# Kernel optimization log

Measured on AMD Instinct MI355X. Metric: run time of the kernel, lower is better.

Reference implementation:

```python
import jax, jax.numpy as jnp
import numpy as np

LMAX = 2
C = 128            # uniform multiplicity per degree
H = 128            # hidden channels
M = (LMAX + 1) ** 2  # 9 spherical coefficients
EPS = 1e-6


def _pack_indices():
    # flat layout per degree block: [mul, 2l+1] channel-major; packed layout: [coeff, channel]
    pack = np.zeros(M * C, dtype=np.int64)
    offset = 0
    for l in range(LMAX + 1):
        dim = 2 * l + 1
        for m in range(dim):
            coeff = l * l + m
            for c in range(C):
                pack[coeff * C + c] = offset + c * dim + m
        offset += C * dim
    unpack = np.argsort(pack)
    return jnp.asarray(pack), jnp.asarray(unpack)

PACK_IDX, UNPACK_IDX = _pack_indices()
# expand_index: degree index for each of the M coefficients
EXPAND_IDX = jnp.asarray(np.repeat(np.arange(LMAX + 1), 2 * np.arange(LMAX + 1) + 1))


def setup_inputs() -> dict:
    key = jax.random.key(0)
    ks = jax.random.split(key, 6)
    N = 10000
    A = 42  # (2*(lmax+1)) * (2*(lmax+1)+1) = 6*7 flattened S2 grid points
    bound = 1.0 / np.sqrt(C)
    return {
        "x": jax.random.normal(ks[0], (N, M * C), dtype=jnp.float32),
        "norm_weight": jnp.ones((LMAX + 1, C), dtype=jnp.float32),
        "w1": jax.random.uniform(ks[1], (LMAX + 1, H, C), jnp.float32, -bound, bound),
        "b1": jnp.zeros((1, 1, H), dtype=jnp.float32),
        "grid_w": jax.random.uniform(ks[2], (2 * H, H), jnp.float32, -bound, bound),
        "grid_b": jnp.zeros((2 * H,), dtype=jnp.float32),
        "w2": jax.random.uniform(ks[3], (LMAX + 1, C, H), jnp.float32, -bound, bound),
        "b2": jnp.zeros((1, 1, C), dtype=jnp.float32),
        "to_grid_mat": jax.random.normal(ks[4], (A, M), dtype=jnp.float32) * 0.3,
        "from_grid_mat": jax.random.normal(ks[5], (M, A), dtype=jnp.float32) * 0.3,
    }


def reference(x, norm_weight, w1, b1, grid_w, grid_b, w2, b2, to_grid_mat, from_grid_mat):
    N = x.shape[0]
    # --- pack flat irreps -> [N, M, C] (pure permutation gather; no padding for uniform irreps)
    p = jnp.take(x, PACK_IDX, axis=1).reshape(N, M, C)
    # --- merged equivariant RMS norm over all (coeff, channel), per-degree-channel affine
    rms = jnp.sqrt(jnp.mean(p * p, axis=(1, 2), keepdims=True) + EPS)
    h = (p / rms) * norm_weight[EXPAND_IDX][None]  # [N, M, C]
    # --- SO3LinearFlat #1: per-degree dense C -> H, bias only on l=0 coeff
    h = jnp.einsum("nmc,mhc->nmh", h, w1[EXPAND_IDX])
    h = h.at[:, 0:1, :].add(b1)
    # --- to S2 grid: [N, M, H] -> [N, A, H]
    g = jnp.einsum("am,nmh->nah", to_grid_mat, h)
    # --- pointwise SwiGLU on grid: H -> 2H linear, silu gate
    z = jnp.einsum("nah,oh->nao", g, grid_w) + grid_b
    g = jax.nn.silu(z[..., :H]) * z[..., H:]
    # --- from S2 grid: [N, A, H] -> [N, M, H]
    h = jnp.einsum("ma,nah->nmh", from_grid_mat, g)
    # --- SO3LinearFlat #2: per-degree dense H -> C, bias only on l=0 coeff
    out = jnp.einsum("nmh,mch->nmc", h, w2[EXPAND_IDX])
    out = out.at[:, 0:1, :].add(b2)
    # --- unpack back to flat irreps layout
    return jnp.take(out.reshape(N, M * C), UNPACK_IDX, axis=1)
```

## Files before the change

### kernel.cpp

```cpp
#include <hip/hip_runtime.h>
#include <math.h>

typedef unsigned short u16;
typedef __attribute__((ext_vector_type(8))) short bf16x8;
typedef __attribute__((ext_vector_type(4))) float f32x4;
typedef __attribute__((ext_vector_type(16))) float f32x16;

constexpr int OFF_W1 = 0;
constexpr int OFF_W2 = 49152;
constexpr int OFF_GW = 98304;
constexpr int OFF_TG = 131072;
constexpr int OFF_FG = 132096;
constexpr int WS_ELEMS = 133632;

__device__ __forceinline__ u16 f2bf(float f) {
    unsigned u = __float_as_uint(f);
    u += 0x7FFFu + ((u >> 16) & 1u);
    return (u16)(u >> 16);
}

__global__ void prep_kernel(const float* __restrict__ w1, const float* __restrict__ gw,
                            const float* __restrict__ w2, const float* __restrict__ tg,
                            const float* __restrict__ fg, u16* __restrict__ wsb) {
    const int idx = blockIdx.x * blockDim.x + threadIdx.x;
    const int str = gridDim.x * blockDim.x;
    for (int i = idx; i < 49152; i += str) wsb[OFF_W1 + i] = f2bf(w1[i]);
    for (int i = idx; i < 49152; i += str) wsb[OFF_W2 + i] = f2bf(w2[i]);
    for (int i = idx; i < 32768; i += str) wsb[OFF_GW + i] = f2bf(gw[i]);
    for (int i = idx; i < 1024; i += str) {
        int a = i >> 4, k = i & 15;
        wsb[OFF_TG + i] = (a < 42 && k < 9) ? f2bf(tg[a * 9 + k]) : (u16)0;
    }
    for (int i = idx; i < 1536; i += str) {
        int m = i / 48, k = i - m * 48;
        wsb[OFF_FG + i] = (m < 9 && k < 42) ? f2bf(fg[m * 42 + k]) : (u16)0;
    }
}

__global__ __launch_bounds__(256, 2) void eqffn_mfma(
    const float* __restrict__ x, const float* __restrict__ nw,
    const float* __restrict__ b1f, const float* __restrict__ gbf,
    const float* __restrict__ b2f, const u16* __restrict__ wsb,
    float* __restrict__ out, int N)
{
    __shared__ u16 sh_a1[64 * 136];
    __shared__ u16 sh_h1T[4 * 128 * 24];
    __shared__ u16 sh_g[48 * 136];
    __shared__ u16 sh_g2T[128 * 56];
    __shared__ float sh_nw[384];
    __shared__ float sh_b1[128];
    __shared__ float sh_b2[128];
    __shared__ float sh_gb[256];

    const int tid  = threadIdx.x;
    const int w    = tid >> 6;
    const int lane = tid & 63;
    const int q    = lane >> 4;
    const int r    = lane & 15;
    const int r32  = lane & 31;
    const int half = lane >> 5;
    const int n0   = blockIdx.x * 4;

    const bf16x8 tgA0 = *(const bf16x8*)&wsb[OFF_TG + r32 * 16 + half * 8];
    const bf16x8 tgA1 = *(const bf16x8*)&wsb[OFF_TG + (32 + r32) * 16 + half * 8];
    bf16x8 fgA[3];
    #pragma unroll
    for (int k = 0; k < 3; ++k)
        fgA[k] = *(const bf16x8*)&wsb[OFF_FG + r32 * 48 + k * 16 + half * 8];
    bf16x8 gwL[2][4], gwH[2][4];
    #pragma unroll
    for (int p = 0; p < 2; ++p) {
        const int oL = (2 * w + p) * 16 + r;
        #pragma unroll
        for (int k = 0; k < 4; ++k) {
            gwL[p][k] = *(const bf16x8*)&wsb[OFF_GW + oL * 128 + k * 32 + q * 8];
            gwH[p][k] = *(const bf16x8*)&wsb[OFF_GW + (oL + 128) * 128 + k * 32 + q * 8];
        }
    }

    for (int i = tid; i < 384; i += 256) sh_nw[i] = nw[i];
    if (tid < 128) { sh_b1[tid] = b1f[tid]; sh_b2[tid] = b2f[tid]; }
    sh_gb[tid] = gbf[tid];
    {
        unsigned long long* z1 = (unsigned long long*)sh_h1T;
        for (int i = tid; i < 3072; i += 256) z1[i] = 0ull;
        unsigned long long* z2 = (unsigned long long*)sh_g2T;
        for (int i = tid; i < 1792; i += 256) z2[i] = 0ull;
    }
    __syncthreads();

    const int myn = n0 + w;
    float4 xv[5];
    float ss = 0.f;
    if (myn < N) {
        const float4* xr = (const float4*)(x + (size_t)myn * 1152);
        for (int i = lane, c2 = 0; i < 288; i += 64, ++c2) {
            float4 v = xr[i]; xv[c2] = v;
            ss += v.x * v.x + v.y * v.y + v.z * v.z + v.w * v.w;
        }
    }
    #pragma unroll
    for (int off = 32; off; off >>= 1) ss += __shfl_xor(ss, off);
    const float inv = 1.0f / sqrtf(ss * (1.0f / 1152.0f) + 1e-6f);
    if (myn < N) {
        for (int i = lane, c2 = 0; i < 288; i += 64, ++c2) {
            float4 v = xv[c2];
            #pragma unroll
            for (int e = 0; e < 4; ++e) {
                const int f = i * 4 + e;
                const float val = ((const float*)&v)[e] * inv;
                int row, c, l;
                if (f < 128)      { l = 0; c = f;            row = w; }
                else if (f < 512) { int t = f - 128; l = 1; c = t / 3; row = 16 + w * 3 + (t - c * 3); }
                else              { int t = f - 512; l = 2; c = t / 5; row = 32 + w * 5 + (t - c * 5); }
                sh_a1[row * 136 + c] = f2bf(val * sh_nw[l * 128 + c]);
            }
        }
    }
    __syncthreads();

    {
        f32x4 acc[4][2];
        #pragma unroll
        for (int a = 0; a < 4; ++a)
            #pragma unroll
            for (int b = 0; b < 2; ++b)
                #pragma unroll
                for (int e = 0; e < 4; ++e) acc[a][b][e] = 0.f;
        #pragma unroll
        for (int mt = 0; mt < 4; ++mt) {
            const int l = (mt == 0) ? 0 : ((mt == 1) ? 1 : 2);
            #pragma unroll
            for (int k = 0; k < 4; ++k) {
                bf16x8 af = *(const bf16x8*)&sh_a1[(mt * 16 + r) * 136 + k * 32 + q * 8];
                #pragma unroll
                for (int nt = 0; nt < 2; ++nt) {
                    const int h = (2 * w + nt) * 16 + r;
                    bf16x8 bf = *(const bf16x8*)&wsb[OFF_W1 + (l * 128 + h) * 128 + k * 32 + q * 8];
                    acc[mt][nt] = __builtin_amdgcn_mfma_f32_16x16x32_bf16(af, bf, acc[mt][nt], 0, 0, 0);
                }
            }
        }
        #pragma unroll
        for (int mt = 0; mt < 4; ++mt) {
            #pragma unroll
            for (int nt = 0; nt < 2; ++nt) {
                const int h = (2 * w + nt) * 16 + r;
                #pragma unroll
                for (int rg = 0; rg < 4; ++rg) {
                    const int rr = q * 4 + rg;
                    const float v = acc[mt][nt][rg];
                    if (mt == 0) {
                        if (rr < 4) sh_h1T[(rr * 128 + h) * 24 + 0] = f2bf(v + sh_b1[h]);
                    } else if (mt == 1) {
                        if (rr < 12) { int nd = rr / 3, mm = rr - nd * 3; sh_h1T[(nd * 128 + h) * 24 + 1 + mm] = f2bf(v); }
                    } else {
                        int rr2 = (mt - 2) * 16 + rr;
                        if (rr2 < 20) { int nd = rr2 / 5, mm = rr2 - nd * 5; sh_h1T[(nd * 128 + h) * 24 + 4 + mm] = f2bf(v); }
                    }
                }
            }
        }
    }
    __syncthreads();

    for (int nn = 0; nn < 4; ++nn) {
        {
            bf16x8 bfn = *(const bf16x8*)&sh_h1T[(nn * 128 + w * 32 + r32) * 24 + half * 8];
            f32x16 ac0, ac1;
            #pragma unroll
            for (int e = 0; e < 16; ++e) { ac0[e] = 0.f; ac1[e] = 0.f; }
            ac0 = __builtin_amdgcn_mfma_f32_32x32x16_bf16(tgA0, bfn, ac0, 0, 0, 0);
            ac1 = __builtin_amdgcn_mfma_f32_32x32x16_bf16(tgA1, bfn, ac1, 0, 0, 0);
            const int h = w * 32 + r32;
            #pragma unroll
            for (int rg = 0; rg < 16; ++rg) {
                const int ar = (rg & 3) + 8 * (rg >> 2) + 4 * half;
                sh_g[ar * 136 + h] = f2bf(ac0[rg]);
                const int ar1 = 32 + ar;
                if (ar1 < 48) sh_g[ar1 * 136 + h] = f2bf(ac1[rg]);
            }
        }
        __syncthreads();

        bf16x8 bfr[3][4];
        #pragma unroll
        for (int nt = 0; nt < 3; ++nt)
            #pragma unroll
            for (int k = 0; k < 4; ++k)
                bfr[nt][k] = *(const bf16x8*)&sh_g[(nt * 16 + r) * 136 + k * 32 + q * 8];
        __syncthreads();

        f32x4 aL[2][3], aH[2][3];
        #pragma unroll
        for (int p = 0; p < 2; ++p)
            #pragma unroll
            for (int nt = 0; nt < 3; ++nt)
                #pragma unroll
                for (int e = 0; e < 4; ++e) { aL[p][nt][e] = 0.f; aH[p][nt][e] = 0.f; }
        #pragma unroll
        for (int p = 0; p < 2; ++p) {
            #pragma unroll
            for (int k = 0; k < 4; ++k) {
                #pragma unroll
                for (int nt = 0; nt < 3; ++nt) {
                    aL[p][nt] = __builtin_amdgcn_mfma_f32_16x16x32_bf16(gwL[p][k], bfr[nt][k], aL[p][nt], 0, 0, 0);
                    aH[p][nt] = __builtin_amdgcn_mfma_f32_16x16x32_bf16(gwH[p][k], bfr[nt][k], aH[p][nt], 0, 0, 0);
                }
            }
        }
        #pragma unroll
        for (int p = 0; p < 2; ++p) {
            #pragma unroll
            for (int nt = 0; nt < 3; ++nt) {
                #pragma unroll
                for (int rg = 0; rg < 4; ++rg) {
                    const int o = (2 * w + p) * 16 + q * 4 + rg;
                    const int a = nt * 16 + r;
                    const float zl = aL[p][nt][rg] + sh_gb[o];
                    const float zh = aH[p][nt][rg] + sh_gb[128 + o];
                    const float gv = zl * (1.0f / (1.0f + __expf(-zl))) * zh;
                    if (a < 42) sh_g2T[o * 56 + a] = f2bf(gv);
                }
            }
        }

        {
            f32x16 ac;
            #pragma unroll
            for (int e = 0; e < 16; ++e) ac[e] = 0.f;
            const int h = w * 32 + r32;
            #pragma unroll
            for (int k = 0; k < 3; ++k) {
                bf16x8 bv = *(const bf16x8*)&sh_g2T[h * 56 + k * 16 + half * 8];
                ac = __builtin_amdgcn_mfma_f32_32x32x16_bf16(fgA[k], bv, ac, 0, 0, 0);
            }
            #pragma unroll
            for (int rg = 0; rg < 16; ++rg) {
                const int m = (rg & 3) + 8 * (rg >> 2) + 4 * half;
                if (m < 9) {
                    const int row = (m == 0) ? nn : ((m < 4) ? (16 + nn * 3 + (m - 1)) : (32 + nn * 5 + (m - 4)));
                    sh_a1[row * 136 + h] = f2bf(ac[rg]);
                }
            }
        }
    }
    __syncthreads();

    {
        f32x4 acc[4][2];
        #pragma unroll
        for (int a = 0; a < 4; ++a)
            #pragma unroll
            for (int b = 0; b < 2; ++b)
                #pragma unroll
                for (int e = 0; e < 4; ++e) acc[a][b][e] = 0.f;
        #pragma unroll
        for (int mt = 0; mt < 4; ++mt) {
            const int l = (mt == 0) ? 0 : ((mt == 1) ? 1 : 2);
            #pragma unroll
            for (int k = 0; k < 4; ++k) {
                bf16x8 af = *(const bf16x8*)&sh_a1[(mt * 16 + r) * 136 + k * 32 + q * 8];
                #pragma unroll
                for (int nt = 0; nt < 2; ++nt) {
                    const int c = (2 * w + nt) * 16 + r;
                    bf16x8 bf = *(const bf16x8*)&wsb[OFF_W2 + (l * 128 + c) * 128 + k * 32 + q * 8];
                    acc[mt][nt] = __builtin_amdgcn_mfma_f32_16x16x32_bf16(af, bf, acc[mt][nt], 0, 0, 0);
                }
            }
        }
        #pragma unroll
        for (int mt = 0; mt < 4; ++mt) {
            #pragma unroll
            for (int nt = 0; nt < 2; ++nt) {
                const int c = (2 * w + nt) * 16 + r;
                #pragma unroll
                for (int rg = 0; rg < 4; ++rg) {
                    const int rr = q * 4 + rg;
                    const float v = acc[mt][nt][rg];
                    if (mt == 0) {
                        if (rr < 4) { int gn = n0 + rr; if (gn < N) out[(size_t)gn * 1152 + c] = v + sh_b2[c]; }
                    } else if (mt == 1) {
                        if (rr < 12) { int nd = rr / 3, mm = rr - nd * 3; int gn = n0 + nd;
                                       if (gn < N) out[(size_t)gn * 1152 + 128 + c * 3 + mm] = v; }
                    } else {
                        int rr2 = (mt - 2) * 16 + rr;
                        if (rr2 < 20) { int nd = rr2 / 5, mm = rr2 - nd * 5; int gn = n0 + nd;
                                        if (gn < N) out[(size_t)gn * 1152 + 512 + c * 5 + mm] = v; }
                    }
                }
            }
        }
    }
}

extern "C" void kernel_launch(void* const* d_in, const int* in_sizes, int n_in,
                              void* d_out, int out_size, void* d_ws, size_t ws_size,
                              hipStream_t stream)
{
    const float* x  = (const float*)d_in[0];
    const float* nw = (const float*)d_in[1];
    const float* w1 = (const float*)d_in[2];
    const float* b1 = (const float*)d_in[3];
    const float* gw = (const float*)d_in[4];
    const float* gb = (const float*)d_in[5];
    const float* w2 = (const float*)d_in[6];
    const float* b2 = (const float*)d_in[7];
    const float* tg = (const float*)d_in[8];
    const float* fg = (const float*)d_in[9];
    float* out = (float*)d_out;
    u16* wsb = (u16*)d_ws;

    const int N = in_sizes[0] / 1152;
    prep_kernel<<<64, 256, 0, stream>>>(w1, gw, w2, tg, fg, wsb);
    eqffn_mfma<<<(N + 3) / 4, 256, 0, stream>>>(x, nw, b1, gb, b2, wsb, out, N);
}
```

Before: 257.1 us.

## Shrink LDS and register footprint to run three blocks per CU

Raises the launch-bounds occupancy target from 2 to 3 blocks per CU. To make that fit, the staging buffer for the first linear's output (sh_h1T) shrinks to a single node slice. The first-linear accumulators now stay in registers and one node's slice is written per loop iteration. The grid SwiGLU weights are no longer held in registers for the whole kernel; they are reloaded from global memory inside each node iteration. This trades repeated cached weight loads and a longer-lived accumulator for more concurrent waves to hide latency.

```diff
diff --git a/kernel.cpp b/kernel.cpp
--- a/kernel.cpp
+++ b/kernel.cpp
@@ -37,14 +37,14 @@
     }
 }
 
-__global__ __launch_bounds__(256, 2) void eqffn_mfma(
+__global__ __launch_bounds__(256, 3) void eqffn_mfma(
     const float* __restrict__ x, const float* __restrict__ nw,
     const float* __restrict__ b1f, const float* __restrict__ gbf,
     const float* __restrict__ b2f, const u16* __restrict__ wsb,
     float* __restrict__ out, int N)
 {
     __shared__ u16 sh_a1[64 * 136];
-    __shared__ u16 sh_h1T[4 * 128 * 24];
+    __shared__ u16 sh_h1T[128 * 20];
     __shared__ u16 sh_g[48 * 136];
     __shared__ u16 sh_g2T[128 * 56];
     __shared__ float sh_nw[384];
@@ -67,23 +67,13 @@
     #pragma unroll
     for (int k = 0; k < 3; ++k)
         fgA[k] = *(const bf16x8*)&wsb[OFF_FG + r32 * 48 + k * 16 + half * 8];
-    bf16x8 gwL[2][4], gwH[2][4];
-    #pragma unroll
-    for (int p = 0; p < 2; ++p) {
-        const int oL = (2 * w + p) * 16 + r;
-        #pragma unroll
-        for (int k = 0; k < 4; ++k) {
-            gwL[p][k] = *(const bf16x8*)&wsb[OFF_GW + oL * 128 + k * 32 + q * 8];
-            gwH[p][k] = *(const bf16x8*)&wsb[OFF_GW + (oL + 128) * 128 + k * 32 + q * 8];
-        }
-    }
 
     for (int i = tid; i < 384; i += 256) sh_nw[i] = nw[i];
     if (tid < 128) { sh_b1[tid] = b1f[tid]; sh_b2[tid] = b2f[tid]; }
     sh_gb[tid] = gbf[tid];
     {
         unsigned long long* z1 = (unsigned long long*)sh_h1T;
-        for (int i = tid; i < 3072; i += 256) z1[i] = 0ull;
+        for (int i = tid; i < 640; i += 256) z1[i] = 0ull;
         unsigned long long* z2 = (unsigned long long*)sh_g2T;
         for (int i = tid; i < 1792; i += 256) z2[i] = 0ull;
     }
@@ -119,14 +109,14 @@
     }
     __syncthreads();
 
+    f32x4 acc1[4][2];
     {
-        f32x4 acc[4][2];
         #pragma unroll
         for (int a = 0; a < 4; ++a)
             #pragma unroll
             for (int b = 0; b < 2; ++b)
                 #pragma unroll
-                for (int e = 0; e < 4; ++e) acc[a][b][e] = 0.f;
+                for (int e = 0; e < 4; ++e) acc1[a][b][e] = 0.f;
         #pragma unroll
         for (int mt = 0; mt < 4; ++mt) {
             const int l = (mt == 0) ? 0 : ((mt == 1) ? 1 : 2);
@@ -137,10 +127,13 @@
                 for (int nt = 0; nt < 2; ++nt) {
                     const int h = (2 * w + nt) * 16 + r;
                     bf16x8 bf = *(const bf16x8*)&wsb[OFF_W1 + (l * 128 + h) * 128 + k * 32 + q * 8];
-                    acc[mt][nt] = __builtin_amdgcn_mfma_f32_16x16x32_bf16(af, bf, acc[mt][nt], 0, 0, 0);
-                }
-            }
-        }
+                    acc1[mt][nt] = __builtin_amdgcn_mfma_f32_16x16x32_bf16(af, bf, acc1[mt][nt], 0, 0, 0);
+                }
+            }
+        }
+    }
+
+    for (int nn = 0; nn < 4; ++nn) {
         #pragma unroll
         for (int mt = 0; mt < 4; ++mt) {
             #pragma unroll
@@ -149,24 +142,21 @@
                 #pragma unroll
                 for (int rg = 0; rg < 4; ++rg) {
                     const int rr = q * 4 + rg;
-                    const float v = acc[mt][nt][rg];
+                    const float v = acc1[mt][nt][rg];
                     if (mt == 0) {
-                        if (rr < 4) sh_h1T[(rr * 128 + h) * 24 + 0] = f2bf(v + sh_b1[h]);
+                        if (rr == nn) sh_h1T[h * 20 + 0] = f2bf(v + sh_b1[h]);
                     } else if (mt == 1) {
-                        if (rr < 12) { int nd = rr / 3, mm = rr - nd * 3; sh_h1T[(nd * 128 + h) * 24 + 1 + mm] = f2bf(v); }
+                        if (rr >= 3 * nn && rr < 3 * nn + 3) sh_h1T[h * 20 + 1 + (rr - 3 * nn)] = f2bf(v);
                     } else {
-                        int rr2 = (mt - 2) * 16 + rr;
-                        if (rr2 < 20) { int nd = rr2 / 5, mm = rr2 - nd * 5; sh_h1T[(nd * 128 + h) * 24 + 4 + mm] = f2bf(v); }
+                        const int rr2 = (mt - 2) * 16 + rr;
+                        if (rr2 >= 5 * nn && rr2 < 5 * nn + 5) sh_h1T[h * 20 + 4 + (rr2 - 5 * nn)] = f2bf(v);
                     }
                 }
             }
         }
-    }
-    __syncthreads();
-
-    for (int nn = 0; nn < 4; ++nn) {
+
         {
-            bf16x8 bfn = *(const bf16x8*)&sh_h1T[(nn * 128 + w * 32 + r32) * 24 + half * 8];
+            bf16x8 bfn = *(const bf16x8*)&sh_h1T[(w * 32 + r32) * 20 + half * 8];
             f32x16 ac0, ac1;
             #pragma unroll
             for (int e = 0; e < 16; ++e) { ac0[e] = 0.f; ac1[e] = 0.f; }
@@ -200,12 +190,15 @@
                 for (int e = 0; e < 4; ++e) { aL[p][nt][e] = 0.f; aH[p][nt][e] = 0.f; }
         #pragma unroll
         for (int p = 0; p < 2; ++p) {
+            const int oL = (2 * w + p) * 16 + r;
             #pragma unroll
             for (int k = 0; k < 4; ++k) {
+                bf16x8 fL = *(const bf16x8*)&wsb[OFF_GW + oL * 128 + k * 32 + q * 8];
+                bf16x8 fH = *(const bf16x8*)&wsb[OFF_GW + (oL + 128) * 128 + k * 32 + q * 8];
                 #pragma unroll
                 for (int nt = 0; nt < 3; ++nt) {
-                    aL[p][nt] = __builtin_amdgcn_mfma_f32_16x16x32_bf16(gwL[p][k], bfr[nt][k], aL[p][nt], 0, 0, 0);
-                    aH[p][nt] = __builtin_amdgcn_mfma_f32_16x16x32_bf16(gwH[p][k], bfr[nt][k], aH[p][nt], 0, 0, 0);
+                    aL[p][nt] = __builtin_amdgcn_mfma_f32_16x16x32_bf16(fL, bfr[nt][k], aL[p][nt], 0, 0, 0);
+                    aH[p][nt] = __builtin_amdgcn_mfma_f32_16x16x32_bf16(fH, bfr[nt][k], aH[p][nt], 0, 0, 0);
                 }
             }
         }
```

New measurement: 384.3 us. 1.49x slower.

## Process two nodes per grid-stage iteration with double-buffered grid tile

Applied to the files above, without the earlier changes.

The per-node S2-grid loop is restructured to handle two nodes per iteration. The grid tile buffer is doubled, so the SwiGLU GEMM runs over both nodes between a single barrier pair, and the barrier after the first linear layer is removed because each wave only reads its own rows. Grid weights are no longer held in registers for the whole kernel; they are reloaded from global memory per k-slice, which frees registers at the cost of extra cached loads. LDS row strides for the intermediate buffers are shrunk, which saves shared memory but makes some 16-byte LDS reads misaligned.

```diff
diff --git a/kernel.cpp b/kernel.cpp
--- a/kernel.cpp
+++ b/kernel.cpp
@@ -44,9 +44,9 @@
     float* __restrict__ out, int N)
 {
     __shared__ u16 sh_a1[64 * 136];
-    __shared__ u16 sh_h1T[4 * 128 * 24];
-    __shared__ u16 sh_g[48 * 136];
-    __shared__ u16 sh_g2T[128 * 56];
+    __shared__ u16 sh_h1T[4 * 128 * 20];
+    __shared__ u16 sh_g[2][48 * 136];
+    __shared__ u16 sh_g2T[128 * 52];
     __shared__ float sh_nw[384];
     __shared__ float sh_b1[128];
     __shared__ float sh_b2[128];
@@ -67,25 +67,15 @@
     #pragma unroll
     for (int k = 0; k < 3; ++k)
         fgA[k] = *(const bf16x8*)&wsb[OFF_FG + r32 * 48 + k * 16 + half * 8];
-    bf16x8 gwL[2][4], gwH[2][4];
-    #pragma unroll
-    for (int p = 0; p < 2; ++p) {
-        const int oL = (2 * w + p) * 16 + r;
-        #pragma unroll
-        for (int k = 0; k < 4; ++k) {
-            gwL[p][k] = *(const bf16x8*)&wsb[OFF_GW + oL * 128 + k * 32 + q * 8];
-            gwH[p][k] = *(const bf16x8*)&wsb[OFF_GW + (oL + 128) * 128 + k * 32 + q * 8];
-        }
-    }
 
     for (int i = tid; i < 384; i += 256) sh_nw[i] = nw[i];
     if (tid < 128) { sh_b1[tid] = b1f[tid]; sh_b2[tid] = b2f[tid]; }
     sh_gb[tid] = gbf[tid];
     {
         unsigned long long* z1 = (unsigned long long*)sh_h1T;
-        for (int i = tid; i < 3072; i += 256) z1[i] = 0ull;
+        for (int i = tid; i < 2560; i += 256) z1[i] = 0ull;
         unsigned long long* z2 = (unsigned long long*)sh_g2T;
-        for (int i = tid; i < 1792; i += 256) z2[i] = 0ull;
+        for (int i = tid; i < 1664; i += 256) z2[i] = 0ull;
     }
     __syncthreads();
 
@@ -151,22 +141,23 @@
                     const int rr = q * 4 + rg;
                     const float v = acc[mt][nt][rg];
                     if (mt == 0) {
-                        if (rr < 4) sh_h1T[(rr * 128 + h) * 24 + 0] = f2bf(v + sh_b1[h]);
+                        if (rr < 4) sh_h1T[(rr * 128 + h) * 20 + 0] = f2bf(v + sh_b1[h]);
                     } else if (mt == 1) {
-                        if (rr < 12) { int nd = rr / 3, mm = rr - nd * 3; sh_h1T[(nd * 128 + h) * 24 + 1 + mm] = f2bf(v); }
+                        if (rr < 12) { int nd = rr / 3, mm = rr - nd * 3; sh_h1T[(nd * 128 + h) * 20 + 1 + mm] = f2bf(v); }
                     } else {
                         int rr2 = (mt - 2) * 16 + rr;
-                        if (rr2 < 20) { int nd = rr2 / 5, mm = rr2 - nd * 5; sh_h1T[(nd * 128 + h) * 24 + 4 + mm] = f2bf(v); }
-                    }
-                }
-            }
-        }
-    }
-    __syncthreads();
-
-    for (int nn = 0; nn < 4; ++nn) {
-        {
-            bf16x8 bfn = *(const bf16x8*)&sh_h1T[(nn * 128 + w * 32 + r32) * 24 + half * 8];
+                        if (rr2 < 20) { int nd = rr2 / 5, mm = rr2 - nd * 5; sh_h1T[(nd * 128 + h) * 20 + 4 + mm] = f2bf(v); }
+                    }
+                }
+            }
+        }
+    }
+
+    for (int it = 0; it < 2; ++it) {
+        #pragma unroll
+        for (int j = 0; j < 2; ++j) {
+            const int nn = 2 * it + j;
+            bf16x8 bfn = *(const bf16x8*)&sh_h1T[(nn * 128 + w * 32 + r32) * 20 + half * 8];
             f32x16 ac0, ac1;
             #pragma unroll
             for (int e = 0; e < 16; ++e) { ac0[e] = 0.f; ac1[e] = 0.f; }
@@ -176,71 +167,82 @@
             #pragma unroll
             for (int rg = 0; rg < 16; ++rg) {
                 const int ar = (rg & 3) + 8 * (rg >> 2) + 4 * half;
-                sh_g[ar * 136 + h] = f2bf(ac0[rg]);
+                sh_g[j][ar * 136 + h] = f2bf(ac0[rg]);
                 const int ar1 = 32 + ar;
-                if (ar1 < 48) sh_g[ar1 * 136 + h] = f2bf(ac1[rg]);
+                if (ar1 < 48) sh_g[j][ar1 * 136 + h] = f2bf(ac1[rg]);
             }
         }
         __syncthreads();
 
-        bf16x8 bfr[3][4];
-        #pragma unroll
-        for (int nt = 0; nt < 3; ++nt)
-            #pragma unroll
-            for (int k = 0; k < 4; ++k)
-                bfr[nt][k] = *(const bf16x8*)&sh_g[(nt * 16 + r) * 136 + k * 32 + q * 8];
-        __syncthreads();
-
-        f32x4 aL[2][3], aH[2][3];
-        #pragma unroll
-        for (int p = 0; p < 2; ++p)
-            #pragma unroll
-            for (int nt = 0; nt < 3; ++nt)
-                #pragma unroll
-                for (int e = 0; e < 4; ++e) { aL[p][nt][e] = 0.f; aH[p][nt][e] = 0.f; }
-        #pragma unroll
-        for (int p = 0; p < 2; ++p) {
-            #pragma unroll
-            for (int k = 0; k < 4; ++k) {
+        f32x4 sL[2][2][3], sH[2][2][3];
+        #pragma unroll
+        for (int j = 0; j < 2; ++j)
+            #pragma unroll
+            for (int p = 0; p < 2; ++p)
+                #pragma unroll
+                for (int nt = 0; nt < 3; ++nt)
+                    #pragma unroll
+                    for (int e = 0; e < 4; ++e) { sL[j][p][nt][e] = 0.f; sH[j][p][nt][e] = 0.f; }
+        #pragma unroll
+        for (int k = 0; k < 4; ++k) {
+            bf16x8 bk[2][3];
+            #pragma unroll
+            for (int j = 0; j < 2; ++j)
+                #pragma unroll
+                for (int nt = 0; nt < 3; ++nt)
+                    bk[j][nt] = *(const bf16x8*)&sh_g[j][(nt * 16 + r) * 136 + k * 32 + q * 8];
+            #pragma unroll
+            for (int p = 0; p < 2; ++p) {
+                const int oL = (2 * w + p) * 16 + r;
+                bf16x8 fL = *(const bf16x8*)&wsb[OFF_GW + oL * 128 + k * 32 + q * 8];
+                bf16x8 fH = *(const bf16x8*)&wsb[OFF_GW + (oL + 128) * 128 + k * 32 + q * 8];
+                #pragma unroll
+                for (int j = 0; j < 2; ++j) {
+                    #pragma unroll
+                    for (int nt = 0; nt < 3; ++nt) {
+                        sL[j][p][nt] = __builtin_amdgcn_mfma_f32_16x16x32_bf16(fL, bk[j][nt], sL[j][p][nt], 0, 0, 0);
+                        sH[j][p][nt] = __builtin_amdgcn_mfma_f32_16x16x32_bf16(fH, bk[j][nt], sH[j][p][nt], 0, 0, 0);
+                    }
+                }
+            }
+        }
+        if (it == 0) __syncthreads();
+
+        #pragma unroll
+        for (int j = 0; j < 2; ++j) {
+            const int nn = 2 * it + j;
+            #pragma unroll
+            for (int p = 0; p < 2; ++p) {
                 #pragma unroll
                 for (int nt = 0; nt < 3; ++nt) {
-                    aL[p][nt] = __builtin_amdgcn_mfma_f32_16x16x32_bf16(gwL[p][k], bfr[nt][k], aL[p][nt], 0, 0, 0);
-                    aH[p][nt] = __builtin_amdgcn_mfma_f32_16x16x32_bf16(gwH[p][k], bfr[nt][k], aH[p][nt], 0, 0, 0);
-                }
-            }
-        }
-        #pragma unroll
-        for (int p = 0; p < 2; ++p) {
-            #pragma unroll
-            for (int nt = 0; nt < 3; ++nt) {
-                #pragma unroll
-                for (int rg = 0; rg < 4; ++rg) {
-                    const int o = (2 * w + p) * 16 + q * 4 + rg;
-                    const int a = nt * 16 + r;
-                    const float zl = aL[p][nt][rg] + sh_gb[o];
-                    const float zh = aH[p][nt][rg] + sh_gb[128 + o];
-                    const float gv = zl * (1.0f / (1.0f + __expf(-zl))) * zh;
-                    if (a < 42) sh_g2T[o * 56 + a] = f2bf(gv);
-                }
-            }
-        }
-
-        {
-            f32x16 ac;
-            #pragma unroll
-            for (int e = 0; e < 16; ++e) ac[e] = 0.f;
-            const int h = w * 32 + r32;
-            #pragma unroll
-            for (int k = 0; k < 3; ++k) {
-                bf16x8 bv = *(const bf16x8*)&sh_g2T[h * 56 + k * 16 + half * 8];
-                ac = __builtin_amdgcn_mfma_f32_32x32x16_bf16(fgA[k], bv, ac, 0, 0, 0);
-            }
-            #pragma unroll
-            for (int rg = 0; rg < 16; ++rg) {
-                const int m = (rg & 3) + 8 * (rg >> 2) + 4 * half;
-                if (m < 9) {
-                    const int row = (m == 0) ? nn : ((m < 4) ? (16 + nn * 3 + (m - 1)) : (32 + nn * 5 + (m - 4)));
-                    sh_a1[row * 136 + h] = f2bf(ac[rg]);
+                    #pragma unroll
+                    for (int rg = 0; rg < 4; ++rg) {
+                        const int o = (2 * w + p) * 16 + q * 4 + rg;
+                        const int a = nt * 16 + r;
+                        const float zl = sL[j][p][nt][rg] + sh_gb[o];
+                        const float zh = sH[j][p][nt][rg] + sh_gb[128 + o];
+                        const float gv = zl * (1.0f / (1.0f + __expf(-zl))) * zh;
+                        if (a < 42) sh_g2T[o * 52 + a] = f2bf(gv);
+                    }
+                }
+            }
+            {
+                f32x16 ac;
+                #pragma unroll
+                for (int e = 0; e < 16; ++e) ac[e] = 0.f;
+                const int h = w * 32 + r32;
+                #pragma unroll
+                for (int k = 0; k < 3; ++k) {
+                    bf16x8 bv = *(const bf16x8*)&sh_g2T[h * 52 + k * 16 + half * 8];
+                    ac = __builtin_amdgcn_mfma_f32_32x32x16_bf16(fgA[k], bv, ac, 0, 0, 0);
+                }
+                #pragma unroll
+                for (int rg = 0; rg < 16; ++rg) {
+                    const int m = (rg & 3) + 8 * (rg >> 2) + 4 * half;
+                    if (m < 9) {
+                        const int row = (m == 0) ? nn : ((m < 4) ? (16 + nn * 3 + (m - 1)) : (32 + nn * 5 + (m - 4)));
+                        sh_a1[row * 136 + h] = f2bf(ac[rg]);
+                    }
                 }
             }
         }
```

Result: no change. 257.5 us (+0.2%).
